# Kernel optimization log

Measured on AMD Instinct MI355X. Metric: run time of the kernel, lower is better.

The kernel has to match this reference:

```python
import jax, jax.numpy as jnp
import numpy as np

D_MODEL = 768

def setup_inputs() -> dict:
    key = jax.random.key(0)
    k1, k2, k3, k4 = jax.random.split(key, 4)
    x = jax.random.normal(k1, (2, 2048, D_MODEL), dtype=jnp.float32)
    w_qkv = jax.random.normal(k2, (3 * D_MODEL, D_MODEL), dtype=jnp.float32) * (1.0 / np.sqrt(D_MODEL))
    w_fc = jax.random.normal(k3, (D_MODEL, D_MODEL), dtype=jnp.float32) * (1.0 / np.sqrt(D_MODEL))
    b_fc = jax.random.normal(k4, (D_MODEL,), dtype=jnp.float32) * 0.01
    return {"x": x, "w_qkv": w_qkv, "w_fc": w_fc, "b_fc": b_fc, "n_head": 12}


def reference(x, w_qkv, w_fc, b_fc, n_head):
    b, n, d = x.shape
    h = int(n_head)
    d_k = d // h
    temperature = float(d_k) ** 0.5  # NOTE: source MULTIPLIES by sqrt(d_k)
    qkv = x @ w_qkv.T                                  # [b, n, 3d] (qkv_bias=False)
    # rearrange 'b n (qkv d h) -> qkv b h n d' : split order is (qkv, d_k, h)
    qkv = qkv.reshape(b, n, 3, d_k, h).transpose(2, 0, 4, 1, 3)  # [3, b, h, n, d_k]
    q, k, v = qkv[0], qkv[1], qkv[2]
    attn = jnp.einsum('bhid,bhjd->bhij', q, k) * temperature      # [b, h, n, n]
    attn = jax.nn.softmax(attn, axis=-1)                           # dropout p=0 -> identity
    out = jnp.einsum('bhij,bhjd->bhid', attn, v)                   # [b, h, n, d_k]
    out = out.transpose(0, 2, 1, 3).reshape(b, n, d)               # 'b h n d -> b n (h d)'
    out = out @ w_fc.T + b_fc                                      # fc (dropout p=0 -> identity)
    return out
```

## Files before the change

### kernel.cpp

```cpp
#include <hip/hip_runtime.h>
#include <stdint.h>

typedef float f32x4 __attribute__((ext_vector_type(4)));
typedef _Float16 f16;
typedef f16 f16x8 __attribute__((ext_vector_type(8)));
typedef f16 f16x4 __attribute__((ext_vector_type(4)));

#define MFMA16(a, b, c) __builtin_amdgcn_mfma_f32_16x16x32_f16((a), (b), (c), 0, 0, 0)

typedef __attribute__((address_space(1))) const uint32_t gu32;
typedef __attribute__((address_space(3))) uint32_t lu32;
__device__ __forceinline__ void gload_lds16(const void* g, void* l) {
    __builtin_amdgcn_global_load_lds((gu32*)g, (lu32*)l, 16, 0, 0);
}

__device__ __forceinline__ size_t kv_elem(int bh, int n, int d) {
    const int kt = n >> 6, row = n & 63;
    return ((size_t)(bh * 32 + kt)) * 4096 + row * 64 + (((d >> 3) ^ (row & 7)) << 3) + (d & 7);
}

__global__ void split_inputs(const float* __restrict__ X, const float* __restrict__ Wq,
                             const float* __restrict__ Wf,
                             f16* __restrict__ Xh, f16* __restrict__ Xl,
                             f16* __restrict__ Wh, f16* __restrict__ Wfb) {
    const int tid = blockIdx.x * 256 + threadIdx.x;
    if (tid < 393216) {
        const float* s = X + (size_t)tid * 8;
        f16 hi[8], lo[8];
#pragma unroll
        for (int j = 0; j < 8; j += 4) {
            f32x4 v = *(const f32x4*)(s + j);
#pragma unroll
            for (int q = 0; q < 4; ++q) {
                f16 h = (f16)v[q];
                hi[j + q] = h;
                lo[j + q] = (f16)(v[q] - (float)h);
            }
        }
        *(f16x8*)(Xh + (size_t)tid * 8) = *(f16x8*)hi;
        *(f16x8*)(Xl + (size_t)tid * 8) = *(f16x8*)lo;
    } else if (tid < 614400) {
        const int t2 = tid - 393216;
        const int row = t2 / 96;
        const int k = (t2 % 96) * 8;
        const int c = row / 768;
        const int rem = row - c * 768;
        const int d = rem / 12;
        const int h2 = rem - d * 12;
        const int cp = c * 768 + h2 * 64 + d;
        const float* s = Wq + (size_t)row * 768 + k;
        f16 hi[8];
#pragma unroll
        for (int j = 0; j < 8; j += 4) {
            f32x4 v = *(const f32x4*)(s + j);
#pragma unroll
            for (int q = 0; q < 4; ++q) hi[j + q] = (f16)v[q];
        }
        *(f16x8*)(Wh + (size_t)cp * 768 + k) = *(f16x8*)hi;
    } else {
        const int t2 = tid - 614400;
        const float* s = Wf + (size_t)t2 * 8;
        f16 hi[8];
#pragma unroll
        for (int j = 0; j < 8; j += 4) {
            f32x4 v = *(const f32x4*)(s + j);
#pragma unroll
            for (int q = 0; q < 4; ++q) hi[j + q] = (f16)v[q];
        }
        *(f16x8*)(Wfb + (size_t)t2 * 8) = *(f16x8*)hi;
    }
}

__global__ __launch_bounds__(256) void qkv_gemm(
    const f16* __restrict__ Xh, const f16* __restrict__ Xl,
    const f16* __restrict__ Wh,
    f16* __restrict__ Qh, f16* __restrict__ Ql,
    f16* __restrict__ Khg, f16* __restrict__ Vb) {
    __shared__ f16 Ah[128 * 32], Al[128 * 32], Bh[128 * 32];
    const int t = threadIdx.x;
    const int lane = t & 63, wv = t >> 6;
    const int wm = (wv >> 1) * 64, wn = (wv & 1) * 64;
    const int r = lane & 15, g = lane >> 4;
    const int bm = blockIdx.x, bn = blockIdx.y;
    const bool full = (bn < 12);

    const int lrow = lane >> 2;
    const int lk = (lane & 3) * 8;

    f32x4 acc[4][4];
#pragma unroll
    for (int i = 0; i < 4; ++i)
#pragma unroll
        for (int j = 0; j < 4; ++j) acc[i][j] = (f32x4)0.0f;

    for (int ks = 0; ks < 768; ks += 32) {
#pragma unroll
        for (int hh = 0; hh < 2; ++hh) {
            const int ii = wv * 2 + hh;
            const int grow = ii * 16 + lrow;
            const size_t ga = (size_t)(bm * 128 + grow) * 768 + ks + lk;
            const size_t gb = (size_t)(bn * 128 + grow) * 768 + ks + lk;
            const int lbase = ii * 512;
            gload_lds16(Xh + ga, &Ah[lbase]);
            gload_lds16(Wh + gb, &Bh[lbase]);
            if (full) gload_lds16(Xl + ga, &Al[lbase]);
        }
        __syncthreads();

        f16x8 a_h[4], b[4];
#pragma unroll
        for (int mf = 0; mf < 4; ++mf) a_h[mf] = *(f16x8*)&Ah[(wm + mf * 16 + r) * 32 + g * 8];
#pragma unroll
        for (int nf = 0; nf < 4; ++nf) b[nf] = *(f16x8*)&Bh[(wn + nf * 16 + r) * 32 + g * 8];
        if (full) {
            f16x8 a_l[4];
#pragma unroll
            for (int mf = 0; mf < 4; ++mf) a_l[mf] = *(f16x8*)&Al[(wm + mf * 16 + r) * 32 + g * 8];
#pragma unroll
            for (int mf = 0; mf < 4; ++mf)
#pragma unroll
                for (int nf = 0; nf < 4; ++nf) {
                    acc[mf][nf] = MFMA16(a_h[mf], b[nf], acc[mf][nf]);
                    acc[mf][nf] = MFMA16(a_l[mf], b[nf], acc[mf][nf]);
                }
        } else {
#pragma unroll
            for (int mf = 0; mf < 4; ++mf)
#pragma unroll
                for (int nf = 0; nf < 4; ++nf)
                    acc[mf][nf] = MFMA16(a_h[mf], b[nf], acc[mf][nf]);
        }
        __syncthreads();
    }

    const int comp = bn / 6;
#pragma unroll
    for (int mf = 0; mf < 4; ++mf)
#pragma unroll
        for (int nf = 0; nf < 4; ++nf) {
            const int col = bn * 128 + wn + nf * 16 + r;
            const int h = (col >> 6) % 12;
            const int d = col & 63;
#pragma unroll
            for (int v = 0; v < 4; ++v) {
                const int row = bm * 128 + wm + mf * 16 + g * 4 + v;
                const int b2 = row >> 11, n = row & 2047;
                const int bh = b2 * 12 + h;
                float val = acc[mf][nf][v];
                if (comp == 0) {
                    const size_t dest = ((size_t)bh * 2048 + n) * 64 + d;
                    val *= 8.0f;
                    f16 hi = (f16)val;
                    Qh[dest] = hi;
                    Ql[dest] = (f16)(val - (float)hi);
                } else if (comp == 1) {
                    Khg[kv_elem(bh, n, d)] = (f16)val;
                } else {
                    Vb[((size_t)bh * 2048 + n) * 64 + d] = (f16)val;
                }
            }
        }
}

__global__ void v_transpose(const f16* __restrict__ Vb, f16* __restrict__ VTg) {
    __shared__ f16 Vt[64 * 72];
    const int t = threadIdx.x;
    const int tile = blockIdx.x;
    const f16* src = Vb + (size_t)tile * 4096;
    const int row = t >> 2, d0 = (t & 3) * 16;
    *(f16x8*)&Vt[row * 72 + d0]     = *(const f16x8*)(src + row * 64 + d0);
    *(f16x8*)&Vt[row * 72 + d0 + 8] = *(const f16x8*)(src + row * 64 + d0 + 8);
    __syncthreads();
    f16* dst = VTg + (size_t)tile * 4096;
#pragma unroll
    for (int it = 0; it < 2; ++it) {
        const int c = t + it * 256;
        const int d = c >> 3, sg = c & 7;
        const int kv0 = (sg ^ (d & 7)) * 8;
        f16 o[8];
#pragma unroll
        for (int j = 0; j < 8; ++j) o[j] = Vt[(kv0 + j) * 72 + d];
        *(f16x8*)(dst + (size_t)c * 8) = *(f16x8*)o;
    }
}

__global__ __launch_bounds__(256, 6) void attn_partial(
    const f16* __restrict__ Qh, const f16* __restrict__ Ql,
    const f16* __restrict__ Khg, const f16* __restrict__ VTg,
    f16* __restrict__ OP, float* __restrict__ Mst, float* __restrict__ Lst) {
    __shared__ f16 Khs[4096], VTs[4096];
    __shared__ f16 Pl[4][16 * 72];

    const int t = threadIdx.x;
    const int lane = t & 63, wv = t >> 6;
    const int r = lane & 15, g = lane >> 4;
    const int bid = blockIdx.x;
    const int half = bid & 1;
    const int qb = (bid >> 1) & 31;
    const int bh = bid >> 6;
    const size_t headoff = (size_t)bh * 2048 * 64;
    const int q0 = qb * 64 + wv * 16;

    f16x8 qh[2], ql[2];
#pragma unroll
    for (int kc = 0; kc < 2; ++kc) {
        const size_t off = headoff + (size_t)(q0 + r) * 64 + kc * 32 + g * 8;
        qh[kc] = *(const f16x8*)(Qh + off);
        ql[kc] = *(const f16x8*)(Ql + off);
    }

    f32x4 o_acc[4];
    float m_run = -1e30f, l_run = 0.0f;
#pragma unroll
    for (int df = 0; df < 4; ++df) o_acc[df] = (f32x4)0.0f;

    for (int kt = half * 16; kt < half * 16 + 16; ++kt) {
        const size_t tb = ((size_t)bh * 32 + kt) * 4096;
#pragma unroll
        for (int c2 = 0; c2 < 2; ++c2) {
            const int c = wv * 2 + c2;
            const int go = c * 512 + lane * 8;
            gload_lds16(Khg + tb + go, &Khs[c * 512]);
            gload_lds16(VTg + tb + go, &VTs[c * 512]);
        }
        __syncthreads();

        f32x4 s[4];
#pragma unroll
        for (int cf = 0; cf < 4; ++cf) s[cf] = (f32x4)0.0f;
#pragma unroll
        for (int kc = 0; kc < 2; ++kc) {
            const int swz = (((kc * 4 + g) ^ (r & 7)) << 3);
            f16x8 ka[4];
#pragma unroll
            for (int cf = 0; cf < 4; ++cf) ka[cf] = *(f16x8*)&Khs[(cf * 16 + r) * 64 + swz];
#pragma unroll
            for (int cf = 0; cf < 4; ++cf) {
                s[cf] = MFMA16(ka[cf], qh[kc], s[cf]);
                s[cf] = MFMA16(ka[cf], ql[kc], s[cf]);
            }
        }

        float mx = -1e30f;
#pragma unroll
        for (int cf = 0; cf < 4; ++cf)
#pragma unroll
            for (int v = 0; v < 4; ++v) mx = fmaxf(mx, s[cf][v]);
        mx = fmaxf(mx, __shfl_xor(mx, 16));
        mx = fmaxf(mx, __shfl_xor(mx, 32));
        const float mn = fmaxf(m_run, mx);
        const float sc = __expf(m_run - mn);
        m_run = mn;
        float rs = 0.0f;
        f16 p16[4][4];
#pragma unroll
        for (int cf = 0; cf < 4; ++cf)
#pragma unroll
            for (int v = 0; v < 4; ++v) {
                const float p = __expf(s[cf][v] - mn);
                rs += p;
                p16[cf][v] = (f16)p;
            }
        rs += __shfl_xor(rs, 16);
        rs += __shfl_xor(rs, 32);
        l_run = l_run * sc + rs;

#pragma unroll
        for (int v = 0; v < 4; ++v) {
            const float scv = __shfl(sc, g * 4 + v);
#pragma unroll
            for (int df = 0; df < 4; ++df) o_acc[df][v] *= scv;
        }

#pragma unroll
        for (int cf = 0; cf < 4; ++cf)
            *(f16x4*)&Pl[wv][r * 72 + cf * 16 + g * 4] = *(f16x4*)p16[cf];

        asm volatile("s_waitcnt lgkmcnt(0)" ::: "memory");
        __builtin_amdgcn_sched_barrier(0);

#pragma unroll
        for (int kc = 0; kc < 2; ++kc) {
            f16x8 pa = *(f16x8*)&Pl[wv][r * 72 + kc * 32 + g * 8];
            const int swz = (((kc * 4 + g) ^ (r & 7)) << 3);
#pragma unroll
            for (int df = 0; df < 4; ++df) {
                f16x8 vb = *(f16x8*)&VTs[(df * 16 + r) * 64 + swz];
                o_acc[df] = MFMA16(pa, vb, o_acc[df]);
            }
        }
        __syncthreads();
    }

    const int pb = (bh << 1) + half;
    if (g == 0) {
        Mst[pb * 2048 + q0 + r] = m_run;
        Lst[pb * 2048 + q0 + r] = l_run;
    }
#pragma unroll
    for (int df = 0; df < 4; ++df)
#pragma unroll
        for (int v = 0; v < 4; ++v) {
            const int n = q0 + g * 4 + v;
            OP[((size_t)pb * 2048 + n) * 64 + df * 16 + r] = (f16)o_acc[df][v];
        }
}

__global__ void attn_combine(const f16* __restrict__ OP, const float* __restrict__ Mst,
                             const float* __restrict__ Lst, f16* __restrict__ AO) {
    const int tid = blockIdx.x * 256 + threadIdx.x;
    const int d4 = (tid & 15) * 4;
    const int pr = tid >> 4;
    const int bh = pr >> 11, n = pr & 2047;
    const int i1 = (bh * 2) * 2048 + n, i2 = i1 + 2048;
    const float m1 = Mst[i1], m2 = Mst[i2];
    const float l1 = Lst[i1], l2 = Lst[i2];
    const float m = fmaxf(m1, m2);
    const float w1 = __expf(m1 - m), w2 = __expf(m2 - m);
    const float inv = 1.0f / (w1 * l1 + w2 * l2);
    f16x4 o1 = *(const f16x4*)(OP + (size_t)i1 * 64 + d4);
    f16x4 o2 = *(const f16x4*)(OP + (size_t)i2 * 64 + d4);
    const int b = bh / 12, h = bh - b * 12;
    f16 out[4];
#pragma unroll
    for (int j = 0; j < 4; ++j)
        out[j] = (f16)((w1 * (float)o1[j] + w2 * (float)o2[j]) * inv);
    *(f16x4*)(AO + ((size_t)(b * 2048 + n)) * 768 + h * 64 + d4) = *(f16x4*)out;
}

__global__ __launch_bounds__(256) void fc_gemm(const f16* __restrict__ A,
                                               const f16* __restrict__ Wfb,
                                               const float* __restrict__ bias,
                                               float* __restrict__ OUT) {
    __shared__ f16 As[64 * 64], Bs[64 * 64];
    const int t = threadIdx.x;
    const int lane = t & 63, wv = t >> 6;
    const int wm = (wv >> 1) * 32, wn = (wv & 1) * 32;
    const int r = lane & 15, g = lane >> 4;
    const int bm = blockIdx.x, bn = blockIdx.y;

    f32x4 acc[2][2];
#pragma unroll
    for (int i = 0; i < 2; ++i)
#pragma unroll
        for (int j = 0; j < 2; ++j) acc[i][j] = (f32x4)0.0f;

    const int srow = t >> 2;
    const int ssg = (t & 3) * 2;

    for (int ks = 0; ks < 768; ks += 64) {
        const f16* as = A + (size_t)(bm * 64 + srow) * 768 + ks;
        const f16* bs = Wfb + (size_t)(bn * 64 + srow) * 768 + ks;
#pragma unroll
        for (int u = 0; u < 2; ++u) {
            const int sg = ssg + u;
            const int dst = srow * 64 + ((sg ^ (srow & 7)) << 3);
            *(f16x8*)&As[dst] = *(const f16x8*)(as + sg * 8);
            *(f16x8*)&Bs[dst] = *(const f16x8*)(bs + sg * 8);
        }
        __syncthreads();

#pragma unroll
        for (int kc = 0; kc < 2; ++kc) {
            f16x8 a[2], b[2];
#pragma unroll
            for (int mf = 0; mf < 2; ++mf) {
                const int row = wm + mf * 16 + r;
                a[mf] = *(f16x8*)&As[row * 64 + (((kc * 4 + g) ^ (row & 7)) << 3)];
            }
#pragma unroll
            for (int nf = 0; nf < 2; ++nf) {
                const int row = wn + nf * 16 + r;
                b[nf] = *(f16x8*)&Bs[row * 64 + (((kc * 4 + g) ^ (row & 7)) << 3)];
            }
#pragma unroll
            for (int mf = 0; mf < 2; ++mf)
#pragma unroll
                for (int nf = 0; nf < 2; ++nf)
                    acc[mf][nf] = MFMA16(a[mf], b[nf], acc[mf][nf]);
        }
        __syncthreads();
    }

#pragma unroll
    for (int nf = 0; nf < 2; ++nf) {
        const int col = bn * 64 + wn + nf * 16 + r;
        const float bv = bias[col];
#pragma unroll
        for (int mf = 0; mf < 2; ++mf) {
            const int row = bm * 64 + wm + mf * 16 + g * 4;
#pragma unroll
            for (int v = 0; v < 4; ++v)
                OUT[(size_t)(row + v) * 768 + col] = acc[mf][nf][v] + bv;
        }
    }
}

extern "C" void kernel_launch(void* const* d_in, const int* in_sizes, int n_in,
                              void* d_out, int out_size, void* d_ws, size_t ws_size,
                              hipStream_t stream) {
    (void)in_sizes; (void)n_in; (void)out_size; (void)ws_size;
    const float* x     = (const float*)d_in[0];
    const float* w_qkv = (const float*)d_in[1];
    const float* w_fc  = (const float*)d_in[2];
    const float* b_fc  = (const float*)d_in[3];
    float* out = (float*)d_out;

    char* ws = (char*)d_ws;
    f16* Xh  = (f16*)ws;
    f16* Xl  = Xh + 3145728;
    f16* Qh  = Xl + 3145728;
    f16* Ql  = Qh + 3145728;
    f16* Khg = Ql + 3145728;
    f16* Vb  = Khg + 3145728;
    f16* VTg = Vb + 3145728;
    f16* AO  = VTg + 3145728;
    f16* Wh  = AO + 3145728;
    f16* Wfb = Wh + 1769472;
    float* Mst = (float*)(Wfb + 589824);
    float* Lst = Mst + 98304;
    f16* OP = Xh;

    split_inputs<<<2688, 256, 0, stream>>>(x, w_qkv, w_fc, Xh, Xl, Wh, Wfb);
    qkv_gemm<<<dim3(32, 18), 256, 0, stream>>>(Xh, Xl, Wh, Qh, Ql, Khg, Vb);
    v_transpose<<<768, 256, 0, stream>>>(Vb, VTg);
    attn_partial<<<1536, 256, 0, stream>>>(Qh, Ql, Khg, VTg, OP, Mst, Lst);
    attn_combine<<<3072, 256, 0, stream>>>(OP, Mst, Lst, AO);
    fc_gemm<<<dim3(64, 12), 256, 0, stream>>>(AO, Wfb, b_fc, out);
}
```

Before: 141.9 us.

## Process two query fragments per wave, split KV three ways, keep P in registers

Each wave now handles 32 query rows (two 16-row fragments), so every K and V tile loaded into LDS is reused across twice as many queries. The KV dimension is split into three parts instead of two, with the combine kernel merging three partial softmax states. V^T is re-laid out so that the softmax probabilities can feed the PV MFMA directly from registers, removing the per-tile LDS round trip for P and its wait. Register pressure rises (launch bounds drop to 4 blocks per SIMD-occupancy target), the grid shrinks, and the split is uneven (11/11/10 tiles). The workspace is reordered so OP, which aliases Xh, has room for three partials.

Result: slower. 158.7 us (+11.8%).

```diff
diff --git a/kernel.cpp b/kernel.cpp
--- a/kernel.cpp
+++ b/kernel.cpp
@@ -175,46 +175,56 @@
 #pragma unroll
     for (int it = 0; it < 2; ++it) {
         const int c = t + it * 256;
-        const int d = c >> 3, sg = c & 7;
-        const int kv0 = (sg ^ (d & 7)) * 8;
+        const int kc = c >> 8;
+        const int d = (c >> 2) & 63;
+        const int gg = c & 3;
+        const int gl = gg ^ ((d >> 1) & 3);
         f16 o[8];
 #pragma unroll
-        for (int j = 0; j < 8; ++j) o[j] = Vt[(kv0 + j) * 72 + d];
+        for (int j = 0; j < 8; ++j) {
+            const int kv = kc * 32 + (j >> 2) * 16 + gl * 4 + (j & 3);
+            o[j] = Vt[kv * 72 + d];
+        }
         *(f16x8*)(dst + (size_t)c * 8) = *(f16x8*)o;
     }
 }
 
-__global__ __launch_bounds__(256, 6) void attn_partial(
+__global__ __launch_bounds__(256, 4) void attn_partial(
     const f16* __restrict__ Qh, const f16* __restrict__ Ql,
     const f16* __restrict__ Khg, const f16* __restrict__ VTg,
     f16* __restrict__ OP, float* __restrict__ Mst, float* __restrict__ Lst) {
     __shared__ f16 Khs[4096], VTs[4096];
-    __shared__ f16 Pl[4][16 * 72];
 
     const int t = threadIdx.x;
     const int lane = t & 63, wv = t >> 6;
     const int r = lane & 15, g = lane >> 4;
     const int bid = blockIdx.x;
-    const int half = bid & 1;
-    const int qb = (bid >> 1) & 31;
-    const int bh = bid >> 6;
+    const int part = bid % 3;
+    const int qb = (bid / 3) & 15;
+    const int bh = bid / 48;
     const size_t headoff = (size_t)bh * 2048 * 64;
-    const int q0 = qb * 64 + wv * 16;
-
-    f16x8 qh[2], ql[2];
-#pragma unroll
-    for (int kc = 0; kc < 2; ++kc) {
-        const size_t off = headoff + (size_t)(q0 + r) * 64 + kc * 32 + g * 8;
-        qh[kc] = *(const f16x8*)(Qh + off);
-        ql[kc] = *(const f16x8*)(Ql + off);
-    }
-
-    f32x4 o_acc[4];
-    float m_run = -1e30f, l_run = 0.0f;
-#pragma unroll
-    for (int df = 0; df < 4; ++df) o_acc[df] = (f32x4)0.0f;
-
-    for (int kt = half * 16; kt < half * 16 + 16; ++kt) {
+    const int q0w = qb * 128 + wv * 32;
+    const int kt0 = part * 11;
+    const int kt1 = (part == 2) ? 32 : kt0 + 11;
+
+    f16x8 qh[2][2], ql[2][2];
+#pragma unroll
+    for (int qf = 0; qf < 2; ++qf)
+#pragma unroll
+        for (int kc = 0; kc < 2; ++kc) {
+            const size_t off = headoff + (size_t)(q0w + qf * 16 + r) * 64 + kc * 32 + g * 8;
+            qh[qf][kc] = *(const f16x8*)(Qh + off);
+            ql[qf][kc] = *(const f16x8*)(Ql + off);
+        }
+
+    f32x4 o_acc[2][4];
+    float m_run[2] = {-1e30f, -1e30f}, l_run[2] = {0.0f, 0.0f};
+#pragma unroll
+    for (int qf = 0; qf < 2; ++qf)
+#pragma unroll
+        for (int df = 0; df < 4; ++df) o_acc[qf][df] = (f32x4)0.0f;
+
+    for (int kt = kt0; kt < kt1; ++kt) {
         const size_t tb = ((size_t)bh * 32 + kt) * 4096;
 #pragma unroll
         for (int c2 = 0; c2 < 2; ++c2) {
@@ -225,85 +235,90 @@
         }
         __syncthreads();
 
-        f32x4 s[4];
-#pragma unroll
-        for (int cf = 0; cf < 4; ++cf) s[cf] = (f32x4)0.0f;
+        f32x4 s[2][4];
+#pragma unroll
+        for (int qf = 0; qf < 2; ++qf)
+#pragma unroll
+            for (int cf = 0; cf < 4; ++cf) s[qf][cf] = (f32x4)0.0f;
 #pragma unroll
         for (int kc = 0; kc < 2; ++kc) {
-            const int swz = (((kc * 4 + g) ^ (r & 7)) << 3);
             f16x8 ka[4];
 #pragma unroll
-            for (int cf = 0; cf < 4; ++cf) ka[cf] = *(f16x8*)&Khs[(cf * 16 + r) * 64 + swz];
-#pragma unroll
-            for (int cf = 0; cf < 4; ++cf) {
-                s[cf] = MFMA16(ka[cf], qh[kc], s[cf]);
-                s[cf] = MFMA16(ka[cf], ql[kc], s[cf]);
-            }
-        }
-
-        float mx = -1e30f;
-#pragma unroll
-        for (int cf = 0; cf < 4; ++cf)
-#pragma unroll
-            for (int v = 0; v < 4; ++v) mx = fmaxf(mx, s[cf][v]);
-        mx = fmaxf(mx, __shfl_xor(mx, 16));
-        mx = fmaxf(mx, __shfl_xor(mx, 32));
-        const float mn = fmaxf(m_run, mx);
-        const float sc = __expf(m_run - mn);
-        m_run = mn;
-        float rs = 0.0f;
-        f16 p16[4][4];
-#pragma unroll
-        for (int cf = 0; cf < 4; ++cf)
+            for (int cf = 0; cf < 4; ++cf)
+                ka[cf] = *(f16x8*)&Khs[(cf * 16 + r) * 64 + (((kc * 4 + g) ^ (r & 7)) << 3)];
+#pragma unroll
+            for (int cf = 0; cf < 4; ++cf)
+#pragma unroll
+                for (int qf = 0; qf < 2; ++qf) {
+                    s[qf][cf] = MFMA16(ka[cf], qh[qf][kc], s[qf][cf]);
+                    s[qf][cf] = MFMA16(ka[cf], ql[qf][kc], s[qf][cf]);
+                }
+        }
+
+        f16x8 pa[2][2];
+        float sc[2];
+#pragma unroll
+        for (int qf = 0; qf < 2; ++qf) {
+            float mx = -1e30f;
+#pragma unroll
+            for (int cf = 0; cf < 4; ++cf)
+#pragma unroll
+                for (int v = 0; v < 4; ++v) mx = fmaxf(mx, s[qf][cf][v]);
+            mx = fmaxf(mx, __shfl_xor(mx, 16));
+            mx = fmaxf(mx, __shfl_xor(mx, 32));
+            const float mn = fmaxf(m_run[qf], mx);
+            sc[qf] = __expf(m_run[qf] - mn);
+            m_run[qf] = mn;
+            float rs = 0.0f;
+#pragma unroll
+            for (int cf = 0; cf < 4; ++cf)
+#pragma unroll
+                for (int v = 0; v < 4; ++v) {
+                    const float p = __expf(s[qf][cf][v] - mn);
+                    rs += p;
+                    pa[qf][cf >> 1][(cf & 1) * 4 + v] = (f16)p;
+                }
+            rs += __shfl_xor(rs, 16);
+            rs += __shfl_xor(rs, 32);
+            l_run[qf] = l_run[qf] * sc[qf] + rs;
+        }
+#pragma unroll
+        for (int qf = 0; qf < 2; ++qf)
 #pragma unroll
             for (int v = 0; v < 4; ++v) {
-                const float p = __expf(s[cf][v] - mn);
-                rs += p;
-                p16[cf][v] = (f16)p;
-            }
-        rs += __shfl_xor(rs, 16);
-        rs += __shfl_xor(rs, 32);
-        l_run = l_run * sc + rs;
-
-#pragma unroll
-        for (int v = 0; v < 4; ++v) {
-            const float scv = __shfl(sc, g * 4 + v);
-#pragma unroll
-            for (int df = 0; df < 4; ++df) o_acc[df][v] *= scv;
-        }
-
-#pragma unroll
-        for (int cf = 0; cf < 4; ++cf)
-            *(f16x4*)&Pl[wv][r * 72 + cf * 16 + g * 4] = *(f16x4*)p16[cf];
-
-        asm volatile("s_waitcnt lgkmcnt(0)" ::: "memory");
-        __builtin_amdgcn_sched_barrier(0);
-
-#pragma unroll
-        for (int kc = 0; kc < 2; ++kc) {
-            f16x8 pa = *(f16x8*)&Pl[wv][r * 72 + kc * 32 + g * 8];
-            const int swz = (((kc * 4 + g) ^ (r & 7)) << 3);
+                const float scv = __shfl(sc[qf], g * 4 + v);
+#pragma unroll
+                for (int df = 0; df < 4; ++df) o_acc[qf][df][v] *= scv;
+            }
+
+#pragma unroll
+        for (int kc = 0; kc < 2; ++kc)
 #pragma unroll
             for (int df = 0; df < 4; ++df) {
-                f16x8 vb = *(f16x8*)&VTs[(df * 16 + r) * 64 + swz];
-                o_acc[df] = MFMA16(pa, vb, o_acc[df]);
-            }
-        }
-        __syncthreads();
-    }
-
-    const int pb = (bh << 1) + half;
-    if (g == 0) {
-        Mst[pb * 2048 + q0 + r] = m_run;
-        Lst[pb * 2048 + q0 + r] = l_run;
-    }
-#pragma unroll
-    for (int df = 0; df < 4; ++df)
-#pragma unroll
-        for (int v = 0; v < 4; ++v) {
-            const int n = q0 + g * 4 + v;
-            OP[((size_t)pb * 2048 + n) * 64 + df * 16 + r] = (f16)o_acc[df][v];
-        }
+                f16x8 vb = *(f16x8*)&VTs[kc * 2048 + (df * 16 + r) * 32 +
+                                         ((g ^ ((r >> 1) & 3)) << 3)];
+#pragma unroll
+                for (int qf = 0; qf < 2; ++qf)
+                    o_acc[qf][df] = MFMA16(pa[qf][kc], vb, o_acc[qf][df]);
+            }
+        __syncthreads();
+    }
+
+    const int pb = bh * 3 + part;
+#pragma unroll
+    for (int qf = 0; qf < 2; ++qf) {
+        if (g == 0) {
+            Mst[pb * 2048 + q0w + qf * 16 + r] = m_run[qf];
+            Lst[pb * 2048 + q0w + qf * 16 + r] = l_run[qf];
+        }
+#pragma unroll
+        for (int df = 0; df < 4; ++df)
+#pragma unroll
+            for (int v = 0; v < 4; ++v) {
+                const int n = q0w + qf * 16 + g * 4 + v;
+                OP[((size_t)pb * 2048 + n) * 64 + df * 16 + r] = (f16)o_acc[qf][df][v];
+            }
+    }
 }
 
 __global__ void attn_combine(const f16* __restrict__ OP, const float* __restrict__ Mst,
@@ -312,19 +327,19 @@
     const int d4 = (tid & 15) * 4;
     const int pr = tid >> 4;
     const int bh = pr >> 11, n = pr & 2047;
-    const int i1 = (bh * 2) * 2048 + n, i2 = i1 + 2048;
-    const float m1 = Mst[i1], m2 = Mst[i2];
-    const float l1 = Lst[i1], l2 = Lst[i2];
-    const float m = fmaxf(m1, m2);
-    const float w1 = __expf(m1 - m), w2 = __expf(m2 - m);
-    const float inv = 1.0f / (w1 * l1 + w2 * l2);
-    f16x4 o1 = *(const f16x4*)(OP + (size_t)i1 * 64 + d4);
-    f16x4 o2 = *(const f16x4*)(OP + (size_t)i2 * 64 + d4);
+    const int i0 = (bh * 3) * 2048 + n;
+    const float m0 = Mst[i0], m1 = Mst[i0 + 2048], m2 = Mst[i0 + 4096];
+    const float m = fmaxf(fmaxf(m0, m1), m2);
+    const float w0 = __expf(m0 - m), w1 = __expf(m1 - m), w2 = __expf(m2 - m);
+    const float inv = 1.0f / (w0 * Lst[i0] + w1 * Lst[i0 + 2048] + w2 * Lst[i0 + 4096]);
+    f16x4 o0 = *(const f16x4*)(OP + (size_t)i0 * 64 + d4);
+    f16x4 o1 = *(const f16x4*)(OP + (size_t)(i0 + 2048) * 64 + d4);
+    f16x4 o2 = *(const f16x4*)(OP + (size_t)(i0 + 4096) * 64 + d4);
     const int b = bh / 12, h = bh - b * 12;
     f16 out[4];
 #pragma unroll
     for (int j = 0; j < 4; ++j)
-        out[j] = (f16)((w1 * (float)o1[j] + w2 * (float)o2[j]) * inv);
+        out[j] = (f16)((w0 * (float)o0[j] + w1 * (float)o1[j] + w2 * (float)o2[j]) * inv);
     *(f16x4*)(AO + ((size_t)(b * 2048 + n)) * 768 + h * 64 + d4) = *(f16x4*)out;
 }
 
@@ -409,22 +424,22 @@
     char* ws = (char*)d_ws;
     f16* Xh  = (f16*)ws;
     f16* Xl  = Xh + 3145728;
-    f16* Qh  = Xl + 3145728;
+    f16* Vb  = Xl + 3145728;
+    f16* Qh  = Vb + 3145728;
     f16* Ql  = Qh + 3145728;
     f16* Khg = Ql + 3145728;
-    f16* Vb  = Khg + 3145728;
-    f16* VTg = Vb + 3145728;
+    f16* VTg = Khg + 3145728;
     f16* AO  = VTg + 3145728;
     f16* Wh  = AO + 3145728;
     f16* Wfb = Wh + 1769472;
     float* Mst = (float*)(Wfb + 589824);
-    float* Lst = Mst + 98304;
+    float* Lst = Mst + 147456;
     f16* OP = Xh;
 
     split_inputs<<<2688, 256, 0, stream>>>(x, w_qkv, w_fc, Xh, Xl, Wh, Wfb);
     qkv_gemm<<<dim3(32, 18), 256, 0, stream>>>(Xh, Xl, Wh, Qh, Ql, Khg, Vb);
     v_transpose<<<768, 256, 0, stream>>>(Vb, VTg);
-    attn_partial<<<1536, 256, 0, stream>>>(Qh, Ql, Khg, VTg, OP, Mst, Lst);
+    attn_partial<<<1152, 256, 0, stream>>>(Qh, Ql, Khg, VTg, OP, Mst, Lst);
     attn_combine<<<3072, 256, 0, stream>>>(OP, Mst, Lst, AO);
     fc_gemm<<<dim3(64, 12), 256, 0, stream>>>(AO, Wfb, b_fc, out);
 }
```
